# Optimization experiments

Measured on AMD Instinct MI355X. Metric: run time of the kernel, lower is better.

## Reference

```python
import jax, jax.numpy as jnp
import numpy as np

N = 500_000
H = 256
G = 4096
NUM_TIMESTEPS = 2


def setup_inputs() -> dict:
    key = jax.random.key(0)
    ks = jax.random.split(key, 12)
    s = 0.05
    x = jax.random.normal(ks[0], (N, H), dtype=jnp.float32)
    batch = jnp.sort(jax.random.randint(ks[1], (N,), 0, G, dtype=jnp.int64))
    return {
        "x": x,
        "gate_w1": jax.random.normal(ks[2], (H, H), dtype=jnp.float32) * s,
        "gate_b1": jax.random.normal(ks[3], (H,), dtype=jnp.float32) * s,
        "gate_w2": jax.random.normal(ks[4], (1, H), dtype=jnp.float32) * s,
        "gate_b2": jax.random.normal(ks[5], (1,), dtype=jnp.float32) * s,
        "gru_w_ih": jax.random.normal(ks[6], (3 * H, H), dtype=jnp.float32) * s,
        "gru_w_hh": jax.random.normal(ks[7], (3 * H, H), dtype=jnp.float32) * s,
        "gru_b_ih": jax.random.normal(ks[8], (3 * H,), dtype=jnp.float32) * s,
        "gru_b_hh": jax.random.normal(ks[9], (3 * H,), dtype=jnp.float32) * s,
        "batch": batch,
        "num_graphs": G,
    }


def _gru_cell(inp, h, w_ih, w_hh, b_ih, b_hh):
    # torch.nn.GRUCell semantics; gate order [r, z, n]
    gi = inp @ w_ih.T + b_ih
    gh = h @ w_hh.T + b_hh
    i_r, i_z, i_n = jnp.split(gi, 3, axis=-1)
    h_r, h_z, h_n = jnp.split(gh, 3, axis=-1)
    r = jax.nn.sigmoid(i_r + h_r)
    z = jax.nn.sigmoid(i_z + h_z)
    n = jnp.tanh(i_n + r * h_n)
    return (1.0 - z) * n + z * h


def reference(x, gate_w1, gate_b1, gate_w2, gate_b2,
              gru_w_ih, gru_w_hh, gru_b_ih, gru_b_hh,
              batch, num_graphs):
    counts = jax.ops.segment_sum(jnp.ones((x.shape[0],), x.dtype), batch,
                                 num_segments=num_graphs)
    denom = jnp.maximum(counts, 1.0)[:, None]  # empty graphs -> 0 mean

    def mean_pool(v):
        return jax.ops.segment_sum(v, batch, num_segments=num_graphs) / denom

    graph_repr = mean_pool(x)  # (G, H)
    for _ in range(NUM_TIMESTEPS):
        # gather per-node graph context (batch is sorted == node_to_graph)
        gate_input = x + graph_repr[batch]  # (N, H)
        hgate = jax.nn.relu(gate_input @ gate_w1.T + gate_b1)
        gate = jax.nn.sigmoid(hgate @ gate_w2.T + gate_b2)  # (N, 1)
        weighted_x = x * gate
        new_graph_repr = mean_pool(weighted_x)
        graph_repr = _gru_cell(new_graph_repr, graph_repr,
                               gru_w_ih, gru_w_hh, gru_b_ih, gru_b_hh)
        graph_repr = jax.nn.relu(graph_repr)
    return graph_repr
```

## Files before the change

kernel.cpp:

```cpp
#include <hip/hip_runtime.h>
#include <hip/hip_bf16.h>
#include <stdint.h>

#define H 256
#define G 4096
#define TK 32
#define TP0 128
#define TPB 256

typedef __attribute__((ext_vector_type(8))) short bf16x8;
typedef __attribute__((ext_vector_type(4))) float f32x4;
typedef __attribute__((ext_vector_type(2))) float f32x2;

__device__ inline short f2bf(float f){
  union { float f; uint32_t u; } v; v.f = f;
  uint32_t r = (v.u + 0x7FFFu + ((v.u >> 16) & 1u)) >> 16;
  return (short)(uint16_t)r;
}
__device__ inline float bf2f(short s){
  union { float f; uint32_t u; } v; v.u = ((uint32_t)(uint16_t)s) << 16;
  return v.f;
}
__device__ inline uint32_t pk2(float lo, float hi){
  return (uint32_t)(uint16_t)f2bf(lo) | ((uint32_t)(uint16_t)f2bf(hi) << 16);
}
__device__ inline uint32_t pkfp8(float4 v){
  int u = __builtin_amdgcn_cvt_pk_fp8_f32(v.x, v.y, 0, false);
  u = __builtin_amdgcn_cvt_pk_fp8_f32(v.z, v.w, u, true);
  return (uint32_t)u;
}
__device__ inline float sigmoidf_(float x){ return 1.f / (1.f + __expf(-x)); }

__device__ inline void ldsbar(){
  asm volatile("s_waitcnt lgkmcnt(0)" ::: "memory");
  __builtin_amdgcn_s_barrier();
}

__global__ void conv_w(const float* __restrict__ w1, const float* __restrict__ wih,
                       const float* __restrict__ whh,
                       short* __restrict__ o1, short* __restrict__ oih, short* __restrict__ ohh,
                       uint8_t* __restrict__ w1q,
                       float* __restrict__ counts, float* __restrict__ pool){
  int i = blockIdx.x * 256 + threadIdx.x;
  if (i < H*H) o1[i] = f2bf(w1[i]);
  if (i < 3*H*H){ oih[i] = f2bf(wih[i]); ohh[i] = f2bf(whh[i]); }
  if (i < H*H/4){
    float4 v = *(const float4*)(w1 + (size_t)i*4);
    *(uint32_t*)(w1q + (size_t)i*4) = pkfp8(v);
  }
  if (i < G) counts[i] = 0.f;
  for (int j = i; j < G*H; j += 768*256) pool[j] = 0.f;
}

__global__ __launch_bounds__(512) __attribute__((amdgpu_waves_per_eu(2, 8)))
void k0_pool(const float* __restrict__ x, const int* __restrict__ batch,
             float* __restrict__ pool, float* __restrict__ counts,
             uint8_t* __restrict__ xq, float* __restrict__ sgate, int nNodes){
  __shared__ int   ng[TP0];
  __shared__ float Pacc[8][H];
  __shared__ float Cacc[8];
  __shared__ int   spanSh;

  const int t = threadIdx.x;
  const int base = blockIdx.x * TP0;
  const int c4 = (t & 63) * 4;
  const int r0 = (t >> 6) * 16;

  float4 v[16];
  #pragma unroll
  for (int i = 0; i < 16; ++i){
    int node = base + r0 + i;
    if (node < nNodes) v[i] = *(const float4*)(x + (size_t)node*H + c4);
    else v[i] = make_float4(0.f,0.f,0.f,0.f);
  }

  { int gi = blockIdx.x * 512 + t; if (gi < nNodes) sgate[gi] = 0.f; }

  if (t < TP0) ng[t] = (base + t < nNodes) ? batch[base + t] : -1;
  for (int u = t; u < 8*H; u += 512) ((float*)Pacc)[u] = 0.f;
  if (t < 8) Cacc[t] = 0.f;
  __syncthreads();

  if (t == 0){
    int lg = ng[0];
    if (base + TP0 <= nNodes) lg = ng[TP0-1];
    else { for (int i = TP0-1; i > 0; --i){ if (ng[i] >= 0){ lg = ng[i]; break; } } }
    spanSh = (ng[0] >= 0) ? (lg - ng[0]) : -1;
  }

  if (xq){
    #pragma unroll
    for (int i = 0; i < 16; ++i){
      int node = base + r0 + i;
      if (node < nNodes)
        *(uint32_t*)(xq + (size_t)node*H + c4) = pkfp8(v[i]);
    }
  }
  __syncthreads();

  const int g0 = ng[0];
  const bool useLds = (spanSh >= 0) && (spanSh < 8);

  float ax=0.f, ay=0.f, az=0.f, aw=0.f;
  int cur = ng[r0];
  if (cur >= 0){
    #pragma unroll
    for (int i = 0; i < 16; ++i){
      int g = ng[r0 + i];
      if (g < 0) break;
      if (g != cur){
        if (useLds){
          atomicAdd(&Pacc[cur-g0][c4], ax);   atomicAdd(&Pacc[cur-g0][c4+1], ay);
          atomicAdd(&Pacc[cur-g0][c4+2], az); atomicAdd(&Pacc[cur-g0][c4+3], aw);
        } else {
          atomicAdd(&pool[(size_t)cur*H + c4], ax);   atomicAdd(&pool[(size_t)cur*H + c4+1], ay);
          atomicAdd(&pool[(size_t)cur*H + c4+2], az); atomicAdd(&pool[(size_t)cur*H + c4+3], aw);
        }
        ax=ay=az=aw=0.f; cur = g;
      }
      ax += v[i].x; ay += v[i].y; az += v[i].z; aw += v[i].w;
    }
    if (useLds){
      atomicAdd(&Pacc[cur-g0][c4], ax);   atomicAdd(&Pacc[cur-g0][c4+1], ay);
      atomicAdd(&Pacc[cur-g0][c4+2], az); atomicAdd(&Pacc[cur-g0][c4+3], aw);
    } else {
      atomicAdd(&pool[(size_t)cur*H + c4], ax);   atomicAdd(&pool[(size_t)cur*H + c4+1], ay);
      atomicAdd(&pool[(size_t)cur*H + c4+2], az); atomicAdd(&pool[(size_t)cur*H + c4+3], aw);
    }
  }
  if (t < TP0 && ng[t] >= 0){
    if (useLds) atomicAdd(&Cacc[ng[t]-g0], 1.f);
    else        atomicAdd(&counts[ng[t]], 1.f);
  }
  __syncthreads();

  if (useLds){
    int nr = spanSh + 1;
    for (int u = t; u < nr*H; u += 512){
      int r = u >> 8, c = u & 255;
      float vv = Pacc[r][c];
      if (vv != 0.f) atomicAdd(&pool[(size_t)(g0+r)*H + c], vv);
    }
    if (t < nr && Cacc[t] != 0.f) atomicAdd(&counts[g0 + t], Cacc[t]);
  }
}

__global__ __launch_bounds__(256) void kT2(float* __restrict__ pool,
    const float* __restrict__ counts, float* __restrict__ repr,
    const short* __restrict__ w1bf, const float* __restrict__ b1,
    uint32_t* __restrict__ hgp){
  __shared__ short Ar[16][H + 8];
  const int t    = threadIdx.x;
  const int wid  = t >> 6;
  const int lane = t & 63;
  const int l15  = lane & 15;
  const int l4   = lane >> 4;
  const int g0   = blockIdx.x * 16;

  for (int u = t; u < 16*32; u += 256){
    int row = u >> 5, cg = u & 31;
    int c0 = cg * 8;
    int g = g0 + row;
    float cnt = fmaxf(counts[g], 1.f);
    float4* pp = (float4*)(pool + (size_t)g*H + c0);
    float4 p0 = pp[0], p1 = pp[1];
    p0.x/=cnt; p0.y/=cnt; p0.z/=cnt; p0.w/=cnt;
    p1.x/=cnt; p1.y/=cnt; p1.z/=cnt; p1.w/=cnt;
    float4* rp = (float4*)(repr + (size_t)g*H + c0);
    rp[0] = p0; rp[1] = p1;
    pp[0] = make_float4(0.f,0.f,0.f,0.f);
    pp[1] = make_float4(0.f,0.f,0.f,0.f);
    bf16x8 o;
    o[0]=f2bf(p0.x); o[1]=f2bf(p0.y); o[2]=f2bf(p0.z); o[3]=f2bf(p0.w);
    o[4]=f2bf(p1.x); o[5]=f2bf(p1.y); o[6]=f2bf(p1.z); o[7]=f2bf(p1.w);
    *(bf16x8*)(&Ar[row][c0]) = o;
  }
  __syncthreads();

  f32x4 acc[4];
  #pragma unroll
  for (int i = 0; i < 4; ++i) acc[i] = (f32x4){0.f,0.f,0.f,0.f};
  #pragma unroll
  for (int kc = 0; kc < 8; ++kc){
    bf16x8 a = *(bf16x8*)(&Ar[l15][kc*32 + l4*8]);
    #pragma unroll
    for (int nt = 0; nt < 4; ++nt){
      int col = wid*64 + nt*16 + l15;
      bf16x8 b = *(const bf16x8*)(w1bf + (size_t)col*H + kc*32 + l4*8);
      acc[nt] = __builtin_amdgcn_mfma_f32_16x16x32_bf16(a, b, acc[nt], 0, 0, 0);
    }
  }
  const float b1v0 = b1[wid*64 + l15];
  const float b1v1 = b1[wid*64 + 16 + l15];
  const float b1v2 = b1[wid*64 + 32 + l15];
  const float b1v3 = b1[wid*64 + 48 + l15];
  #pragma unroll
  for (int j = 0; j < 4; ++j){
    int row = l4*4 + j;
    hgp[(size_t)(g0+row)*128 + wid*32 + l15]      = pk2(acc[0][j]+b1v0, acc[1][j]+b1v1);
    hgp[(size_t)(g0+row)*128 + wid*32 + 16 + l15] = pk2(acc[2][j]+b1v2, acc[3][j]+b1v3);
  }
}

__global__ __launch_bounds__(256) __attribute__((amdgpu_waves_per_eu(3, 4)))
void k1a_fp8(
    const uint8_t* __restrict__ xq, const int* __restrict__ batch,
    const uint32_t* __restrict__ hgp, const uint8_t* __restrict__ w1q,
    const float* __restrict__ w2, float* __restrict__ sgate,
    int nNodes, int nTiles, int nBlk){

  __shared__ uint8_t Ain[2][TK][H + 16];
  __shared__ int     ngS[2][TK];

  const int t    = threadIdx.x;
  const int wid  = t >> 6;
  const int lane = t & 63;
  const int l15  = lane & 15;
  const int l4   = lane >> 4;
  const int colB = wid*64;

  const int tile0 = (int)(((long long)blockIdx.x * nTiles) / nBlk);
  const int tile1 = (int)(((long long)(blockIdx.x+1) * nTiles) / nBlk);
  if (tile0 >= tile1) return;

  long BfA0[8], BfA1[8], BfB0[8], BfB1[8];
  {
    const uint8_t* wp = w1q + (size_t)(colB + l15)*H + l4*8;
    #pragma unroll
    for (int kc = 0; kc < 8; ++kc){
      BfA0[kc] = *(const long*)(wp + kc*32);
      BfA1[kc] = *(const long*)(wp + 16*H + kc*32);
      BfB0[kc] = *(const long*)(wp + 32*H + kc*32);
      BfB1[kc] = *(const long*)(wp + 48*H + kc*32);
    }
  }
  const float w2A0 = w2[colB + l15];
  const float w2A1 = w2[colB + 16 + l15];
  const float w2B0 = w2[colB + 32 + l15];
  const float w2B1 = w2[colB + 48 + l15];

  const int srow  = t >> 4;
  const int scolB = (t & 15) * 16;
  uint4 xv0, xv1;
  int ngv = -1;

  auto issueT = [&](int tile){
    int base = tile * TK;
    int n0 = base + srow, n1 = n0 + 16;
    xv0 = (n0 < nNodes) ? *(const uint4*)(xq + (size_t)n0*H + scolB) : make_uint4(0,0,0,0);
    xv1 = (n1 < nNodes) ? *(const uint4*)(xq + (size_t)n1*H + scolB) : make_uint4(0,0,0,0);
    if (t < TK){
      int node = base + t;
      ngv = (node < nNodes) ? batch[node] : -1;
    }
  };
  auto stageT = [&](int buf){
    *(uint4*)(&Ain[buf][srow][scolB])      = xv0;
    *(uint4*)(&Ain[buf][srow + 16][scolB]) = xv1;
    if (t < TK) ngS[buf][t] = ngv;
  };

  issueT(tile0);
  stageT(0);
  if (tile0 + 1 < tile1) issueT(tile0 + 1);

  int cur = 0;
  for (int tile = tile0; tile < tile1; ++tile, cur ^= 1){
    ldsbar();

    uint32_t hvp[2][4];
    #pragma unroll
    for (int r = 0; r < 2; ++r)
      #pragma unroll
      for (int j = 0; j < 4; ++j){
        int g = ngS[cur][r*16 + l4*4 + j];
        hvp[r][j] = (g >= 0) ? hgp[(size_t)g*128 + wid*32 + l15] : 0u;
      }

    f32x4 acc0[2], acc1[2];
    #pragma unroll
    for (int r = 0; r < 2; ++r){ acc0[r] = (f32x4){0.f,0.f,0.f,0.f}; acc1[r] = (f32x4){0.f,0.f,0.f,0.f}; }
    #pragma unroll
    for (int kc = 0; kc < 8; ++kc){
      #pragma unroll
      for (int r = 0; r < 2; ++r){
        long a = *(const long*)(&Ain[cur][r*16 + l15][kc*32 + l4*8]);
        acc0[r] = __builtin_amdgcn_mfma_f32_16x16x32_fp8_fp8(a, BfA0[kc], acc0[r], 0, 0, 0);
        acc1[r] = __builtin_amdgcn_mfma_f32_16x16x32_fp8_fp8(a, BfA1[kc], acc1[r], 0, 0, 0);
      }
    }

    if (tile + 1 < tile1){
      stageT(cur ^ 1);
      if (tile + 2 < tile1) issueT(tile + 2);
    }

    float p[2][4];
    #pragma unroll
    for (int r = 0; r < 2; ++r)
      #pragma unroll
      for (int j = 0; j < 4; ++j){
        float h0 = fmaxf(acc0[r][j] + bf2f((short)(uint16_t)(hvp[r][j] & 0xFFFFu)), 0.f);
        float h1 = fmaxf(acc1[r][j] + bf2f((short)(uint16_t)(hvp[r][j] >> 16)), 0.f);
        p[r][j] = w2A0*h0 + w2A1*h1;
      }

    #pragma unroll
    for (int r = 0; r < 2; ++r)
      #pragma unroll
      for (int j = 0; j < 4; ++j){
        int g = ngS[cur][r*16 + l4*4 + j];
        hvp[r][j] = (g >= 0) ? hgp[(size_t)g*128 + wid*32 + 16 + l15] : 0u;
      }
    #pragma unroll
    for (int r = 0; r < 2; ++r){ acc0[r] = (f32x4){0.f,0.f,0.f,0.f}; acc1[r] = (f32x4){0.f,0.f,0.f,0.f}; }
    #pragma unroll
    for (int kc = 0; kc < 8; ++kc){
      #pragma unroll
      for (int r = 0; r < 2; ++r){
        long a = *(const long*)(&Ain[cur][r*16 + l15][kc*32 + l4*8]);
        acc0[r] = __builtin_amdgcn_mfma_f32_16x16x32_fp8_fp8(a, BfB0[kc], acc0[r], 0, 0, 0);
        acc1[r] = __builtin_amdgcn_mfma_f32_16x16x32_fp8_fp8(a, BfB1[kc], acc1[r], 0, 0, 0);
      }
    }
    #pragma unroll
    for (int r = 0; r < 2; ++r)
      #pragma unroll
      for (int j = 0; j < 4; ++j){
        float h0 = fmaxf(acc0[r][j] + bf2f((short)(uint16_t)(hvp[r][j] & 0xFFFFu)), 0.f);
        float h1 = fmaxf(acc1[r][j] + bf2f((short)(uint16_t)(hvp[r][j] >> 16)), 0.f);
        p[r][j] += w2B0*h0 + w2B1*h1;
      }

    #pragma unroll
    for (int off = 1; off < 16; off <<= 1){
      #pragma unroll
      for (int r = 0; r < 2; ++r)
        #pragma unroll
        for (int j = 0; j < 4; ++j) p[r][j] += __shfl_xor(p[r][j], off);
    }
    if (l15 == 0){
      int base = tile * TK;
      #pragma unroll
      for (int r = 0; r < 2; ++r)
        #pragma unroll
        for (int j = 0; j < 4; ++j){
          int idx = r*16 + l4*4 + j;
          if (ngS[cur][idx] >= 0)
            atomicAdd(&sgate[base + idx], p[r][j]);
        }
    }
  }
}

__global__ __launch_bounds__(512) __attribute__((amdgpu_waves_per_eu(2, 8)))
void k1b_q8(
    const uint8_t* __restrict__ xq, const int* __restrict__ batch,
    float* __restrict__ sgate, const float* __restrict__ b2p,
    float* __restrict__ pool, int nNodes){

  __shared__ int   ng[TPB];
  __shared__ float gs[TPB];
  __shared__ float Pacc[8][H];
  __shared__ int   spanSh;

  const int t = threadIdx.x;
  const int base = blockIdx.x * TPB;
  const int c4 = (t & 63) * 4;
  const int r0 = (t >> 6) * 32;

  uint32_t u[32];
  #pragma unroll
  for (int i = 0; i < 32; ++i){
    int node = base + r0 + i;
    u[i] = (node < nNodes) ? *(const uint32_t*)(xq + (size_t)node*H + c4) : 0u;
  }

  const float b2v = b2p[0];
  {
    int node = base + t;
    if (t < TPB){
      if (node < nNodes){
        ng[t] = batch[node];
        gs[t] = sigmoidf_(sgate[node] + b2v);
        sgate[node] = 0.f;
      } else { ng[t] = -1; gs[t] = 0.f; }
    }
  }
  for (int w = t; w < 8*H; w += 512) ((float*)Pacc)[w] = 0.f;
  __syncthreads();

  if (t == 0){
    int lg = ng[0];
    if (base + TPB <= nNodes) lg = ng[TPB-1];
    else { for (int i = TPB-1; i > 0; --i){ if (ng[i] >= 0){ lg = ng[i]; break; } } }
    spanSh = (ng[0] >= 0) ? (lg - ng[0]) : -1;
  }
  __syncthreads();

  const int g0 = ng[0];
  const bool useLds = (spanSh >= 0) && (spanSh < 8);

  float ax=0.f, ay=0.f, az=0.f, aw=0.f;
  int cur = ng[r0];
  if (cur >= 0){
    #pragma unroll
    for (int i = 0; i < 32; ++i){
      int g = ng[r0 + i];
      if (g < 0) break;
      if (g != cur){
        if (useLds){
          atomicAdd(&Pacc[cur-g0][c4], ax);   atomicAdd(&Pacc[cur-g0][c4+1], ay);
          atomicAdd(&Pacc[cur-g0][c4+2], az); atomicAdd(&Pacc[cur-g0][c4+3], aw);
        } else {
          atomicAdd(&pool[(size_t)cur*H + c4], ax);   atomicAdd(&pool[(size_t)cur*H + c4+1], ay);
          atomicAdd(&pool[(size_t)cur*H + c4+2], az); atomicAdd(&pool[(size_t)cur*H + c4+3], aw);
        }
        ax=ay=az=aw=0.f; cur = g;
      }
      float gv = gs[r0 + i];
      f32x2 lo = __builtin_amdgcn_cvt_pk_f32_fp8((int)u[i], false);
      f32x2 hi = __builtin_amdgcn_cvt_pk_f32_fp8((int)u[i], true);
      ax += gv * lo[0]; ay += gv * lo[1];
      az += gv * hi[0]; aw += gv * hi[1];
    }
    if (useLds){
      atomicAdd(&Pacc[cur-g0][c4], ax);   atomicAdd(&Pacc[cur-g0][c4+1], ay);
      atomicAdd(&Pacc[cur-g0][c4+2], az); atomicAdd(&Pacc[cur-g0][c4+3], aw);
    } else {
      atomicAdd(&pool[(size_t)cur*H + c4], ax);   atomicAdd(&pool[(size_t)cur*H + c4+1], ay);
      atomicAdd(&pool[(size_t)cur*H + c4+2], az); atomicAdd(&pool[(size_t)cur*H + c4+3], aw);
    }
  }
  __syncthreads();

  if (useLds){
    int nr = spanSh + 1;
    for (int w = t; w < nr*H; w += 512){
      int r = w >> 8, c = w & 255;
      float vv = Pacc[r][c];
      if (vv != 0.f) atomicAdd(&pool[(size_t)(g0+r)*H + c], vv);
    }
  }
}

__global__ __launch_bounds__(256) __attribute__((amdgpu_waves_per_eu(3, 4)))
void k1a_gate_f32(
    const float* __restrict__ xf32, const int* __restrict__ batch,
    const uint32_t* __restrict__ hgp, const short* __restrict__ w1bf,
    const float* __restrict__ w2, float* __restrict__ sgate,
    int nNodes, int nTiles, int nChains){

  __shared__ short Ain[2][TK][H + 8];
  __shared__ int   ngS[2][TK];

  const int t    = threadIdx.x;
  const int wid  = t >> 6;
  const int lane = t & 63;
  const int l15  = lane & 15;
  const int l4   = lane >> 4;

  const int ch    = blockIdx.x >= nChains;
  const int chain = ch ? blockIdx.x - nChains : blockIdx.x;
  const int colB  = ch*128 + wid*32;
  const int hgcol = ch*64 + wid*16 + l15;

  const int tile0 = (int)(((long long)chain * nTiles) / nChains);
  const int tile1 = (int)(((long long)(chain+1) * nTiles) / nChains);
  if (tile0 >= tile1) return;

  bf16x8 Bf0[8], Bf1[8];
  {
    const short* wp0 = w1bf + (size_t)(colB + l15)*H + l4*8;
    #pragma unroll
    for (int kc = 0; kc < 8; ++kc){
      Bf0[kc] = *(const bf16x8*)(wp0 + kc*32);
      Bf1[kc] = *(const bf16x8*)(wp0 + 16*H + kc*32);
    }
  }
  const float w2v0 = w2[colB + l15];
  const float w2v1 = w2[colB + 16 + l15];

  const int srow = t >> 5;
  const int scol = (t & 31) * 8;
  float4 xf[4][2];
  int ngv = -1;

  auto issueT = [&](int tile){
    int base = tile * TK;
    #pragma unroll
    for (int q = 0; q < 4; ++q){
      int node = base + srow + q*8;
      if (node < nNodes){
        const float4* xp = (const float4*)(xf32 + (size_t)node*H + scol);
        xf[q][0] = xp[0]; xf[q][1] = xp[1];
      } else { xf[q][0] = make_float4(0.f,0.f,0.f,0.f); xf[q][1] = make_float4(0.f,0.f,0.f,0.f); }
    }
    if (t < TK){
      int node = base + t;
      ngv = (node < nNodes) ? batch[node] : -1;
    }
  };
  auto stageT = [&](int buf){
    #pragma unroll
    for (int q = 0; q < 4; ++q){
      bf16x8 o;
      float4 a = xf[q][0], c = xf[q][1];
      o[0]=f2bf(a.x); o[1]=f2bf(a.y); o[2]=f2bf(a.z); o[3]=f2bf(a.w);
      o[4]=f2bf(c.x); o[5]=f2bf(c.y); o[6]=f2bf(c.z); o[7]=f2bf(c.w);
      *(bf16x8*)(&Ain[buf][srow + q*8][scol]) = o;
    }
    if (t < TK) ngS[buf][t] = ngv;
  };

  issueT(tile0);
  stageT(0);
  if (tile0 + 1 < tile1) issueT(tile0 + 1);

  int cur = 0;
  for (int tile = tile0; tile < tile1; ++tile, cur ^= 1){
    ldsbar();

    int gr[2][4];
    uint32_t hvp[2][4];
    #pragma unroll
    for (int r = 0; r < 2; ++r)
      #pragma unroll
      for (int j = 0; j < 4; ++j){
        int g = ngS[cur][r*16 + l4*4 + j];
        gr[r][j] = g;
        hvp[r][j] = (g >= 0) ? hgp[(size_t)g*128 + hgcol] : 0u;
      }

    f32x4 acc0[2], acc1[2];
    #pragma unroll
    for (int r = 0; r < 2; ++r){ acc0[r] = (f32x4){0.f,0.f,0.f,0.f}; acc1[r] = (f32x4){0.f,0.f,0.f,0.f}; }
    #pragma unroll
    for (int kc = 0; kc < 8; ++kc){
      #pragma unroll
      for (int r = 0; r < 2; ++r){
        bf16x8 a = *(bf16x8*)(&Ain[cur][r*16 + l15][kc*32 + l4*8]);
        acc0[r] = __builtin_amdgcn_mfma_f32_16x16x32_bf16(a, Bf0[kc], acc0[r], 0, 0, 0);
        acc1[r] = __builtin_amdgcn_mfma_f32_16x16x32_bf16(a, Bf1[kc], acc1[r], 0, 0, 0);
      }
    }

    if (tile + 1 < tile1){
      stageT(cur ^ 1);
      if (tile + 2 < tile1) issueT(tile + 2);
    }

    float p[2][4];
    #pragma unroll
    for (int r = 0; r < 2; ++r)
      #pragma unroll
      for (int j = 0; j < 4; ++j){
        float h0 = fmaxf(acc0[r][j] + bf2f((short)(uint16_t)(hvp[r][j] & 0xFFFFu)), 0.f);
        float h1 = fmaxf(acc1[r][j] + bf2f((short)(uint16_t)(hvp[r][j] >> 16)), 0.f);
        p[r][j] = w2v0*h0 + w2v1*h1;
      }
    #pragma unroll
    for (int off = 1; off < 16; off <<= 1){
      #pragma unroll
      for (int r = 0; r < 2; ++r)
        #pragma unroll
        for (int j = 0; j < 4; ++j) p[r][j] += __shfl_xor(p[r][j], off);
    }
    if (l15 == 0){
      int base = tile * TK;
      #pragma unroll
      for (int r = 0; r < 2; ++r)
        #pragma unroll
        for (int j = 0; j < 4; ++j){
          if (gr[r][j] >= 0)
            atomicAdd(&sgate[base + r*16 + l4*4 + j], p[r][j]);
        }
    }
  }
}

__global__ __launch_bounds__(512) __attribute__((amdgpu_waves_per_eu(2, 8)))
void k1b_f32(
    const float* __restrict__ xf32, const int* __restrict__ batch,
    float* __restrict__ sgate, const float* __restrict__ b2p,
    float* __restrict__ pool, int nNodes){

  __shared__ int   ng[TP0];
  __shared__ float gs[TP0];
  __shared__ float Pacc[8][H];
  __shared__ int   spanSh;

  const int t = threadIdx.x;
  const int base = blockIdx.x * TP0;
  const int c4 = (t & 63) * 4;
  const int r0 = (t >> 6) * 16;

  float4 vf[16];
  #pragma unroll
  for (int i = 0; i < 16; ++i){
    int node = base + r0 + i;
    vf[i] = (node < nNodes) ? *(const float4*)(xf32 + (size_t)node*H + c4)
                            : make_float4(0.f,0.f,0.f,0.f);
  }

  const float b2v = b2p[0];
  if (t < TP0){
    int node = base + t;
    if (node < nNodes){
      ng[t] = batch[node];
      gs[t] = sigmoidf_(sgate[node] + b2v);
      sgate[node] = 0.f;
    } else { ng[t] = -1; gs[t] = 0.f; }
  }
  for (int w = t; w < 8*H; w += 512) ((float*)Pacc)[w] = 0.f;
  __syncthreads();

  if (t == 0){
    int lg = ng[0];
    if (base + TP0 <= nNodes) lg = ng[TP0-1];
    else { for (int i = TP0-1; i > 0; --i){ if (ng[i] >= 0){ lg = ng[i]; break; } } }
    spanSh = (ng[0] >= 0) ? (lg - ng[0]) : -1;
  }
  __syncthreads();

  const int g0 = ng[0];
  const bool useLds = (spanSh >= 0) && (spanSh < 8);

  float ax=0.f, ay=0.f, az=0.f, aw=0.f;
  int cur = ng[r0];
  if (cur >= 0){
    #pragma unroll
    for (int i = 0; i < 16; ++i){
      int g = ng[r0 + i];
      if (g < 0) break;
      if (g != cur){
        if (useLds){
          atomicAdd(&Pacc[cur-g0][c4], ax);   atomicAdd(&Pacc[cur-g0][c4+1], ay);
          atomicAdd(&Pacc[cur-g0][c4+2], az); atomicAdd(&Pacc[cur-g0][c4+3], aw);
        } else {
          atomicAdd(&pool[(size_t)cur*H + c4], ax);   atomicAdd(&pool[(size_t)cur*H + c4+1], ay);
          atomicAdd(&pool[(size_t)cur*H + c4+2], az); atomicAdd(&pool[(size_t)cur*H + c4+3], aw);
        }
        ax=ay=az=aw=0.f; cur = g;
      }
      float gv = gs[r0 + i];
      ax += gv * bf2f(f2bf(vf[i].x)); ay += gv * bf2f(f2bf(vf[i].y));
      az += gv * bf2f(f2bf(vf[i].z)); aw += gv * bf2f(f2bf(vf[i].w));
    }
    if (useLds){
      atomicAdd(&Pacc[cur-g0][c4], ax);   atomicAdd(&Pacc[cur-g0][c4+1], ay);
      atomicAdd(&Pacc[cur-g0][c4+2], az); atomicAdd(&Pacc[cur-g0][c4+3], aw);
    } else {
      atomicAdd(&pool[(size_t)cur*H + c4], ax);   atomicAdd(&pool[(size_t)cur*H + c4+1], ay);
      atomicAdd(&pool[(size_t)cur*H + c4+2], az); atomicAdd(&pool[(size_t)cur*H + c4+3], aw);
    }
  }
  __syncthreads();

  if (useLds){
    int nr = spanSh + 1;
    for (int w = t; w < nr*H; w += 512){
      int r = w >> 8, c = w & 255;
      float vv = Pacc[r][c];
      if (vv != 0.f) atomicAdd(&pool[(size_t)(g0+r)*H + c], vv);
    }
  }
}

__global__ __launch_bounds__(256) void k2_gru(float* __restrict__ pool,
    const float* __restrict__ counts, const float* __restrict__ repr_in,
    const short* __restrict__ wihbf, const short* __restrict__ whhbf,
    const float* __restrict__ bih, const float* __restrict__ bhh,
    float* __restrict__ repr_out,
    const short* __restrict__ w1bf, const float* __restrict__ b1,
    uint32_t* __restrict__ hgp, int doHg){

  __shared__ short Anew[16][H + 8];
  __shared__ short Aold[16][H + 8];
  __shared__ float hold[16][H];
  __shared__ float srz[16][2*H];
  __shared__ float sni[16][H];
  __shared__ float snh[16][H];

  const int t    = threadIdx.x;
  const int wid  = t >> 6;
  const int lane = t & 63;
  const int l15  = lane & 15;
  const int l4   = lane >> 4;
  const int g0   = blockIdx.x * 16;

  for (int u = t; u < 16*H; u += 256){
    int row = u >> 8, c = u & 255;
    int g = g0 + row;
    float cnt = fmaxf(counts[g], 1.f);
    float rin = repr_in[(size_t)g*H + c];
    float nr  = pool[(size_t)g*H + c] / cnt;
    pool[(size_t)g*H + c] = 0.f;
    Anew[row][c] = f2bf(nr);
    Aold[row][c] = f2bf(rin);
    hold[row][c] = rin;
  }
  __syncthreads();

  f32x4 ai[12], ah[12];
  #pragma unroll
  for (int i = 0; i < 12; ++i){ ai[i] = (f32x4){0.f,0.f,0.f,0.f}; ah[i] = (f32x4){0.f,0.f,0.f,0.f}; }

  for (int kc = 0; kc < 8; ++kc){
    bf16x8 an = *(bf16x8*)(&Anew[l15][kc*32 + l4*8]);
    bf16x8 ao = *(bf16x8*)(&Aold[l15][kc*32 + l4*8]);
    #pragma unroll
    for (int nt = 0; nt < 12; ++nt){
      int n = wid*192 + nt*16 + l15;
      bf16x8 bi = *(const bf16x8*)(wihbf + (size_t)n*H + kc*32 + l4*8);
      bf16x8 bh = *(const bf16x8*)(whhbf + (size_t)n*H + kc*32 + l4*8);
      ai[nt] = __builtin_amdgcn_mfma_f32_16x16x32_bf16(an, bi, ai[nt], 0, 0, 0);
      ah[nt] = __builtin_amdgcn_mfma_f32_16x16x32_bf16(ao, bh, ah[nt], 0, 0, 0);
    }
  }

  #pragma unroll
  for (int nt = 0; nt < 12; ++nt){
    int n = wid*192 + nt*16 + l15;
    float bi = bih[n], bh = bhh[n];
    #pragma unroll
    for (int r = 0; r < 4; ++r){
      int row = l4*4 + r;
      float si = ai[nt][r] + bi;
      float sh = ah[nt][r] + bh;
      if (n < 2*H) srz[row][n] = si + sh;
      else { sni[row][n - 2*H] = si; snh[row][n - 2*H] = sh; }
    }
  }
  __syncthreads();

  for (int u = t; u < 16*H; u += 256){
    int row = u >> 8, c = u & 255;
    float rr = sigmoidf_(srz[row][c]);
    float zz = sigmoidf_(srz[row][H + c]);
    float nn = tanhf(sni[row][c] + rr * snh[row][c]);
    float hv = (1.f - zz) * nn + zz * hold[row][c];
    float out = fmaxf(hv, 0.f);
    repr_out[(size_t)(g0 + row)*H + c] = out;
    Anew[row][c] = f2bf(out);
  }

  if (doHg){
    __syncthreads();
    f32x4 acc[4];
    #pragma unroll
    for (int i = 0; i < 4; ++i) acc[i] = (f32x4){0.f,0.f,0.f,0.f};
    #pragma unroll
    for (int kc = 0; kc < 8; ++kc){
      bf16x8 a = *(bf16x8*)(&Anew[l15][kc*32 + l4*8]);
      #pragma unroll
      for (int nt = 0; nt < 4; ++nt){
        int col = wid*64 + nt*16 + l15;
        bf16x8 b = *(const bf16x8*)(w1bf + (size_t)col*H + kc*32 + l4*8);
        acc[nt] = __builtin_amdgcn_mfma_f32_16x16x32_bf16(a, b, acc[nt], 0, 0, 0);
      }
    }
    const float b1v0 = b1[wid*64 + l15];
    const float b1v1 = b1[wid*64 + 16 + l15];
    const float b1v2 = b1[wid*64 + 32 + l15];
    const float b1v3 = b1[wid*64 + 48 + l15];
    #pragma unroll
    for (int j = 0; j < 4; ++j){
      int row = l4*4 + j;
      hgp[(size_t)(g0+row)*128 + wid*32 + l15]      = pk2(acc[0][j]+b1v0, acc[1][j]+b1v1);
      hgp[(size_t)(g0+row)*128 + wid*32 + 16 + l15] = pk2(acc[2][j]+b1v2, acc[3][j]+b1v3);
    }
  }
}

extern "C" void kernel_launch(void* const* d_in, const int* in_sizes, int n_in,
                              void* d_out, int out_size, void* d_ws, size_t ws_size,
                              hipStream_t stream){
  const float* x    = (const float*)d_in[0];
  const float* w1   = (const float*)d_in[1];
  const float* b1   = (const float*)d_in[2];
  const float* w2   = (const float*)d_in[3];
  const float* b2   = (const float*)d_in[4];
  const float* wih  = (const float*)d_in[5];
  const float* whh  = (const float*)d_in[6];
  const float* bih  = (const float*)d_in[7];
  const float* bhh  = (const float*)d_in[8];
  const int*   batch= (const int*)d_in[9];
  const int N = in_sizes[9];

  char* ws = (char*)d_ws;
  short* w1bf   = (short*)(ws + 0);
  short* wihbf  = (short*)(ws + (1u<<17));
  short* whhbf  = (short*)(ws + (1u<<19));
  float* counts = (float*)(ws + 917504);
  uint8_t* w1q  = (uint8_t*)(ws + 933888);
  float* pool   = (float*)(ws + (1u<<20));
  float* repr   = (float*)(ws + (1u<<20) + (1u<<22));
  float* sgate  = (float*)(ws + (9u<<20));
  uint32_t* hgp = (uint32_t*)(ws + (12u<<20));
  float* outp   = (float*)d_out;

  const size_t XQ_OFF = (size_t)16u << 20;
  const bool useXq = ws_size >= XQ_OFF + (size_t)N * H;
  uint8_t* xq = useXq ? (uint8_t*)(ws + XQ_OFF) : nullptr;

  const int nTiles32 = (N + TK - 1) / TK;
  const int nBlk1a  = 1024;
  const int nChainsF= 512;
  const int nBlkP   = (N + TP0 - 1) / TP0;
  const int nBlkQ   = (N + TPB - 1) / TPB;

  conv_w<<<768, 256, 0, stream>>>(w1, wih, whh, w1bf, wihbf, whhbf, w1q, counts, pool);
  k0_pool<<<nBlkP, 512, 0, stream>>>(x, batch, pool, counts, xq, sgate, N);
  kT2<<<G/16, 256, 0, stream>>>(pool, counts, repr, w1bf, b1, hgp);

  for (int ts = 0; ts < 2; ++ts){
    if (useXq){
      k1a_fp8<<<nBlk1a, 256, 0, stream>>>(xq, batch, hgp, w1q, w2, sgate, N, nTiles32, nBlk1a);
      k1b_q8<<<nBlkQ, 512, 0, stream>>>(xq, batch, sgate, b2, pool, N);
    } else {
      k1a_gate_f32<<<nChainsF*2, 256, 0, stream>>>(x, batch, hgp, w1bf, w2, sgate, N, nTiles32, nChainsF);
      k1b_f32<<<nBlkP, 512, 0, stream>>>(x, batch, sgate, b2, pool, N);
    }
    k2_gru<<<G/16, 256, 0, stream>>>(pool, counts, repr, wihbf, whhbf, bih, bhh,
                                     (ts == 0) ? repr : outp,
                                     w1bf, b1, hgp, (ts == 0) ? 1 : 0);
  }
}
```

Baseline: 588.5 us.

## Precompute x@W1 once and reuse across timesteps via linearity

Uses the linearity of (x + repr[batch]) @ W1^T to compute x@W1^T once per call into a bf16 buffer hx (N×256). Each timestep then adds the per-graph hg term, applies relu and the w2 dot product inside the pooling kernel, so the fp8 MFMA GEMM no longer runs twice. The column layout of hg is changed to interleaved pairs so it matches hx. The cost is a 256 MB bf16 intermediate that is written once and read twice, and a larger workspace requirement that gates whether this path is used at all.

```diff
diff --git a/kernel.cpp b/kernel.cpp
--- a/kernel.cpp
+++ b/kernel.cpp
@@ -148,7 +148,7 @@
 __global__ __launch_bounds__(256) void kT2(float* __restrict__ pool,
     const float* __restrict__ counts, float* __restrict__ repr,
     const short* __restrict__ w1bf, const float* __restrict__ b1,
-    uint32_t* __restrict__ hgp){
+    uint32_t* __restrict__ hgl){
   __shared__ short Ar[16][H + 8];
   const int t    = threadIdx.x;
   const int wid  = t >> 6;
@@ -180,37 +180,33 @@
   f32x4 acc[4];
   #pragma unroll
   for (int i = 0; i < 4; ++i) acc[i] = (f32x4){0.f,0.f,0.f,0.f};
+  const short* bp0 = w1bf + (size_t)(wid*64 + 2*l15)*H;
+  const short* bq0 = w1bf + (size_t)(wid*64 + 32 + 2*l15)*H;
   #pragma unroll
   for (int kc = 0; kc < 8; ++kc){
     bf16x8 a = *(bf16x8*)(&Ar[l15][kc*32 + l4*8]);
-    #pragma unroll
-    for (int nt = 0; nt < 4; ++nt){
-      int col = wid*64 + nt*16 + l15;
-      bf16x8 b = *(const bf16x8*)(w1bf + (size_t)col*H + kc*32 + l4*8);
-      acc[nt] = __builtin_amdgcn_mfma_f32_16x16x32_bf16(a, b, acc[nt], 0, 0, 0);
-    }
-  }
-  const float b1v0 = b1[wid*64 + l15];
-  const float b1v1 = b1[wid*64 + 16 + l15];
-  const float b1v2 = b1[wid*64 + 32 + l15];
-  const float b1v3 = b1[wid*64 + 48 + l15];
+    acc[0] = __builtin_amdgcn_mfma_f32_16x16x32_bf16(a, *(const bf16x8*)(bp0 + kc*32 + l4*8), acc[0], 0, 0, 0);
+    acc[1] = __builtin_amdgcn_mfma_f32_16x16x32_bf16(a, *(const bf16x8*)(bp0 + H + kc*32 + l4*8), acc[1], 0, 0, 0);
+    acc[2] = __builtin_amdgcn_mfma_f32_16x16x32_bf16(a, *(const bf16x8*)(bq0 + kc*32 + l4*8), acc[2], 0, 0, 0);
+    acc[3] = __builtin_amdgcn_mfma_f32_16x16x32_bf16(a, *(const bf16x8*)(bq0 + H + kc*32 + l4*8), acc[3], 0, 0, 0);
+  }
+  const float b1p0 = b1[wid*64 + 2*l15];
+  const float b1p1 = b1[wid*64 + 2*l15 + 1];
+  const float b1q0 = b1[wid*64 + 32 + 2*l15];
+  const float b1q1 = b1[wid*64 + 32 + 2*l15 + 1];
   #pragma unroll
   for (int j = 0; j < 4; ++j){
     int row = l4*4 + j;
-    hgp[(size_t)(g0+row)*128 + wid*32 + l15]      = pk2(acc[0][j]+b1v0, acc[1][j]+b1v1);
-    hgp[(size_t)(g0+row)*128 + wid*32 + 16 + l15] = pk2(acc[2][j]+b1v2, acc[3][j]+b1v3);
+    hgl[(size_t)(g0+row)*128 + wid*32 + l15]      = pk2(acc[0][j]+b1p0, acc[1][j]+b1p1);
+    hgl[(size_t)(g0+row)*128 + wid*32 + 16 + l15] = pk2(acc[2][j]+b1q0, acc[3][j]+b1q1);
   }
 }
 
 __global__ __launch_bounds__(256) __attribute__((amdgpu_waves_per_eu(3, 4)))
-void k1a_fp8(
-    const uint8_t* __restrict__ xq, const int* __restrict__ batch,
-    const uint32_t* __restrict__ hgp, const uint8_t* __restrict__ w1q,
-    const float* __restrict__ w2, float* __restrict__ sgate,
-    int nNodes, int nTiles, int nBlk){
+void kX_hx(const uint8_t* __restrict__ xq, const uint8_t* __restrict__ w1q,
+           uint32_t* __restrict__ hx, int nNodes, int nTiles, int nBlk){
 
   __shared__ uint8_t Ain[2][TK][H + 16];
-  __shared__ int     ngS[2][TK];
 
   const int t    = threadIdx.x;
   const int wid  = t >> 6;
@@ -223,41 +219,32 @@
   const int tile1 = (int)(((long long)(blockIdx.x+1) * nTiles) / nBlk);
   if (tile0 >= tile1) return;
 
-  long BfA0[8], BfA1[8], BfB0[8], BfB1[8];
+  long BfP0[8], BfP1[8], BfQ0[8], BfQ1[8];
   {
-    const uint8_t* wp = w1q + (size_t)(colB + l15)*H + l4*8;
+    const uint8_t* wp = w1q + (size_t)(colB + 2*l15)*H + l4*8;
+    const uint8_t* wq = w1q + (size_t)(colB + 32 + 2*l15)*H + l4*8;
     #pragma unroll
     for (int kc = 0; kc < 8; ++kc){
-      BfA0[kc] = *(const long*)(wp + kc*32);
-      BfA1[kc] = *(const long*)(wp + 16*H + kc*32);
-      BfB0[kc] = *(const long*)(wp + 32*H + kc*32);
-      BfB1[kc] = *(const long*)(wp + 48*H + kc*32);
-    }
-  }
-  const float w2A0 = w2[colB + l15];
-  const float w2A1 = w2[colB + 16 + l15];
-  const float w2B0 = w2[colB + 32 + l15];
-  const float w2B1 = w2[colB + 48 + l15];
+      BfP0[kc] = *(const long*)(wp + kc*32);
+      BfP1[kc] = *(const long*)(wp + H + kc*32);
+      BfQ0[kc] = *(const long*)(wq + kc*32);
+      BfQ1[kc] = *(const long*)(wq + H + kc*32);
+    }
+  }
 
   const int srow  = t >> 4;
   const int scolB = (t & 15) * 16;
   uint4 xv0, xv1;
-  int ngv = -1;
 
   auto issueT = [&](int tile){
     int base = tile * TK;
     int n0 = base + srow, n1 = n0 + 16;
     xv0 = (n0 < nNodes) ? *(const uint4*)(xq + (size_t)n0*H + scolB) : make_uint4(0,0,0,0);
     xv1 = (n1 < nNodes) ? *(const uint4*)(xq + (size_t)n1*H + scolB) : make_uint4(0,0,0,0);
-    if (t < TK){
-      int node = base + t;
-      ngv = (node < nNodes) ? batch[node] : -1;
-    }
   };
   auto stageT = [&](int buf){
     *(uint4*)(&Ain[buf][srow][scolB])      = xv0;
     *(uint4*)(&Ain[buf][srow + 16][scolB]) = xv1;
-    if (t < TK) ngS[buf][t] = ngv;
   };
 
   issueT(tile0);
@@ -267,26 +254,18 @@
   int cur = 0;
   for (int tile = tile0; tile < tile1; ++tile, cur ^= 1){
     ldsbar();
-
-    uint32_t hvp[2][4];
-    #pragma unroll
-    for (int r = 0; r < 2; ++r)
-      #pragma unroll
-      for (int j = 0; j < 4; ++j){
-        int g = ngS[cur][r*16 + l4*4 + j];
-        hvp[r][j] = (g >= 0) ? hgp[(size_t)g*128 + wid*32 + l15] : 0u;
-      }
-
-    f32x4 acc0[2], acc1[2];
-    #pragma unroll
-    for (int r = 0; r < 2; ++r){ acc0[r] = (f32x4){0.f,0.f,0.f,0.f}; acc1[r] = (f32x4){0.f,0.f,0.f,0.f}; }
+    const int nbase = tile * TK;
+
+    f32x4 a0[2], a1[2];
+    #pragma unroll
+    for (int r = 0; r < 2; ++r){ a0[r] = (f32x4){0.f,0.f,0.f,0.f}; a1[r] = (f32x4){0.f,0.f,0.f,0.f}; }
     #pragma unroll
     for (int kc = 0; kc < 8; ++kc){
       #pragma unroll
       for (int r = 0; r < 2; ++r){
         long a = *(const long*)(&Ain[cur][r*16 + l15][kc*32 + l4*8]);
-        acc0[r] = __builtin_amdgcn_mfma_f32_16x16x32_fp8_fp8(a, BfA0[kc], acc0[r], 0, 0, 0);
-        acc1[r] = __builtin_amdgcn_mfma_f32_16x16x32_fp8_fp8(a, BfA1[kc], acc1[r], 0, 0, 0);
+        a0[r] = __builtin_amdgcn_mfma_f32_16x16x32_fp8_fp8(a, BfP0[kc], a0[r], 0, 0, 0);
+        a1[r] = __builtin_amdgcn_mfma_f32_16x16x32_fp8_fp8(a, BfP1[kc], a1[r], 0, 0, 0);
       }
     }
 
@@ -295,72 +274,46 @@
       if (tile + 2 < tile1) issueT(tile + 2);
     }
 
-    float p[2][4];
     #pragma unroll
     for (int r = 0; r < 2; ++r)
       #pragma unroll
       for (int j = 0; j < 4; ++j){
-        float h0 = fmaxf(acc0[r][j] + bf2f((short)(uint16_t)(hvp[r][j] & 0xFFFFu)), 0.f);
-        float h1 = fmaxf(acc1[r][j] + bf2f((short)(uint16_t)(hvp[r][j] >> 16)), 0.f);
-        p[r][j] = w2A0*h0 + w2A1*h1;
-      }
-
-    #pragma unroll
-    for (int r = 0; r < 2; ++r)
-      #pragma unroll
-      for (int j = 0; j < 4; ++j){
-        int g = ngS[cur][r*16 + l4*4 + j];
-        hvp[r][j] = (g >= 0) ? hgp[(size_t)g*128 + wid*32 + 16 + l15] : 0u;
-      }
-    #pragma unroll
-    for (int r = 0; r < 2; ++r){ acc0[r] = (f32x4){0.f,0.f,0.f,0.f}; acc1[r] = (f32x4){0.f,0.f,0.f,0.f}; }
+        int node = nbase + r*16 + l4*4 + j;
+        if (node < nNodes)
+          hx[(size_t)node*128 + wid*32 + l15] = pk2(a0[r][j], a1[r][j]);
+      }
+
+    #pragma unroll
+    for (int r = 0; r < 2; ++r){ a0[r] = (f32x4){0.f,0.f,0.f,0.f}; a1[r] = (f32x4){0.f,0.f,0.f,0.f}; }
     #pragma unroll
     for (int kc = 0; kc < 8; ++kc){
       #pragma unroll
       for (int r = 0; r < 2; ++r){
         long a = *(const long*)(&Ain[cur][r*16 + l15][kc*32 + l4*8]);
-        acc0[r] = __builtin_amdgcn_mfma_f32_16x16x32_fp8_fp8(a, BfB0[kc], acc0[r], 0, 0, 0);
-        acc1[r] = __builtin_amdgcn_mfma_f32_16x16x32_fp8_fp8(a, BfB1[kc], acc1[r], 0, 0, 0);
+        a0[r] = __builtin_amdgcn_mfma_f32_16x16x32_fp8_fp8(a, BfQ0[kc], a0[r], 0, 0, 0);
+        a1[r] = __builtin_amdgcn_mfma_f32_16x16x32_fp8_fp8(a, BfQ1[kc], a1[r], 0, 0, 0);
       }
     }
     #pragma unroll
     for (int r = 0; r < 2; ++r)
       #pragma unroll
       for (int j = 0; j < 4; ++j){
-        float h0 = fmaxf(acc0[r][j] + bf2f((short)(uint16_t)(hvp[r][j] & 0xFFFFu)), 0.f);
-        float h1 = fmaxf(acc1[r][j] + bf2f((short)(uint16_t)(hvp[r][j] >> 16)), 0.f);
-        p[r][j] += w2B0*h0 + w2B1*h1;
-      }
-
-    #pragma unroll
-    for (int off = 1; off < 16; off <<= 1){
-      #pragma unroll
-      for (int r = 0; r < 2; ++r)
-        #pragma unroll
-        for (int j = 0; j < 4; ++j) p[r][j] += __shfl_xor(p[r][j], off);
-    }
-    if (l15 == 0){
-      int base = tile * TK;
-      #pragma unroll
-      for (int r = 0; r < 2; ++r)
-        #pragma unroll
-        for (int j = 0; j < 4; ++j){
-          int idx = r*16 + l4*4 + j;
-          if (ngS[cur][idx] >= 0)
-            atomicAdd(&sgate[base + idx], p[r][j]);
-        }
-    }
+        int node = nbase + r*16 + l4*4 + j;
+        if (node < nNodes)
+          hx[(size_t)node*128 + wid*32 + 16 + l15] = pk2(a0[r][j], a1[r][j]);
+      }
   }
 }
 
 __global__ __launch_bounds__(512) __attribute__((amdgpu_waves_per_eu(2, 8)))
-void k1b_q8(
-    const uint8_t* __restrict__ xq, const int* __restrict__ batch,
-    float* __restrict__ sgate, const float* __restrict__ b2p,
-    float* __restrict__ pool, int nNodes){
+void kG(const uint32_t* __restrict__ hx, const uint32_t* __restrict__ hgl,
+        const uint8_t* __restrict__ xq, const int* __restrict__ batch,
+        const float* __restrict__ w2, const float* __restrict__ b2p,
+        float* __restrict__ pool, int nNodes){
 
   __shared__ int   ng[TPB];
   __shared__ float gs[TPB];
+  __shared__ float w2s[H];
   __shared__ float Pacc[8][H];
   __shared__ int   spanSh;
 
@@ -377,16 +330,12 @@
   }
 
   const float b2v = b2p[0];
-  {
-    int node = base + t;
-    if (t < TPB){
-      if (node < nNodes){
-        ng[t] = batch[node];
-        gs[t] = sigmoidf_(sgate[node] + b2v);
-        sgate[node] = 0.f;
-      } else { ng[t] = -1; gs[t] = 0.f; }
-    }
-  }
+  const int nA = base + (t >> 1);
+  const int half = t & 1;
+  const int gA = (nA < nNodes) ? batch[nA] : -1;
+
+  if (t < H) w2s[t] = w2[t];
+  if (t < TPB) ng[t] = (base + t < nNodes) ? batch[base + t] : -1;
   for (int w = t; w < 8*H; w += 512) ((float*)Pacc)[w] = 0.f;
   __syncthreads();
 
@@ -396,6 +345,23 @@
     else { for (int i = TPB-1; i > 0; --i){ if (ng[i] >= 0){ lg = ng[i]; break; } } }
     spanSh = (ng[0] >= 0) ? (lg - ng[0]) : -1;
   }
+
+  float s = 0.f;
+  if (gA >= 0){
+    const uint32_t* hxp = hx  + (size_t)nA*128 + half*64;
+    const uint32_t* hgp = hgl + (size_t)gA*128 + half*64;
+    #pragma unroll
+    for (int k = 0; k < 64; ++k){
+      uint32_t hxd = hxp[k];
+      uint32_t hgd = hgp[k];
+      float lo = bf2f((short)(uint16_t)(hxd & 0xFFFFu)) + bf2f((short)(uint16_t)(hgd & 0xFFFFu));
+      float hi = bf2f((short)(uint16_t)(hxd >> 16))     + bf2f((short)(uint16_t)(hgd >> 16));
+      int c = half*128 + k*2;
+      s += w2s[c] * fmaxf(lo, 0.f) + w2s[c+1] * fmaxf(hi, 0.f);
+    }
+  }
+  s += __shfl_xor(s, 1);
+  if ((t & 1) == 0) gs[t >> 1] = (gA >= 0) ? sigmoidf_(s + b2v) : 0.f;
   __syncthreads();
 
   const int g0 = ng[0];
@@ -447,7 +413,7 @@
 __global__ __launch_bounds__(256) __attribute__((amdgpu_waves_per_eu(3, 4)))
 void k1a_gate_f32(
     const float* __restrict__ xf32, const int* __restrict__ batch,
-    const uint32_t* __restrict__ hgp, const short* __restrict__ w1bf,
+    const uint32_t* __restrict__ hgl, const short* __restrict__ w1bf,
     const float* __restrict__ w2, float* __restrict__ sgate,
     int nNodes, int nTiles, int nChains){
 
@@ -463,7 +429,7 @@
   const int ch    = blockIdx.x >= nChains;
   const int chain = ch ? blockIdx.x - nChains : blockIdx.x;
   const int colB  = ch*128 + wid*32;
-  const int hgcol = ch*64 + wid*16 + l15;
+  const int sel   = l15 & 1;
 
   const int tile0 = (int)(((long long)chain * nTiles) / nChains);
   const int tile1 = (int)(((long long)(chain+1) * nTiles) / nChains);
@@ -522,14 +488,19 @@
     ldsbar();
 
     int gr[2][4];
-    uint32_t hvp[2][4];
+    float hvA[2][4], hvB[2][4];
     #pragma unroll
     for (int r = 0; r < 2; ++r)
       #pragma unroll
       for (int j = 0; j < 4; ++j){
         int g = ngS[cur][r*16 + l4*4 + j];
         gr[r][j] = g;
-        hvp[r][j] = (g >= 0) ? hgp[(size_t)g*128 + hgcol] : 0u;
+        if (g >= 0){
+          uint32_t dA = hgl[(size_t)g*128 + (colB>>1) + (l15>>1)];
+          uint32_t dB = hgl[(size_t)g*128 + (colB>>1) + 8 + (l15>>1)];
+          hvA[r][j] = bf2f((short)(uint16_t)(sel ? (dA >> 16) : (dA & 0xFFFFu)));
+          hvB[r][j] = bf2f((short)(uint16_t)(sel ? (dB >> 16) : (dB & 0xFFFFu)));
+        } else { hvA[r][j] = 0.f; hvB[r][j] = 0.f; }
       }
 
     f32x4 acc0[2], acc1[2];
@@ -555,8 +526,8 @@
     for (int r = 0; r < 2; ++r)
       #pragma unroll
       for (int j = 0; j < 4; ++j){
-        float h0 = fmaxf(acc0[r][j] + bf2f((short)(uint16_t)(hvp[r][j] & 0xFFFFu)), 0.f);
-        float h1 = fmaxf(acc1[r][j] + bf2f((short)(uint16_t)(hvp[r][j] >> 16)), 0.f);
+        float h0 = fmaxf(acc0[r][j] + hvA[r][j], 0.f);
+        float h1 = fmaxf(acc1[r][j] + hvB[r][j], 0.f);
         p[r][j] = w2v0*h0 + w2v1*h1;
       }
     #pragma unroll
@@ -673,7 +644,7 @@
     const float* __restrict__ bih, const float* __restrict__ bhh,
     float* __restrict__ repr_out,
     const short* __restrict__ w1bf, const float* __restrict__ b1,
-    uint32_t* __restrict__ hgp, int doHg){
+    uint32_t* __restrict__ hgl, int doHg){
 
   __shared__ short Anew[16][H + 8];
   __shared__ short Aold[16][H + 8];
@@ -750,25 +721,25 @@
     f32x4 acc[4];
     #pragma unroll
     for (int i = 0; i < 4; ++i) acc[i] = (f32x4){0.f,0.f,0.f,0.f};
+    const short* bp0 = w1bf + (size_t)(wid*64 + 2*l15)*H;
+    const short* bq0 = w1bf + (size_t)(wid*64 + 32 + 2*l15)*H;
     #pragma unroll
     for (int kc = 0; kc < 8; ++kc){
       bf16x8 a = *(bf16x8*)(&Anew[l15][kc*32 + l4*8]);
-      #pragma unroll
-      for (int nt = 0; nt < 4; ++nt){
-        int col = wid*64 + nt*16 + l15;
-        bf16x8 b = *(const bf16x8*)(w1bf + (size_t)col*H + kc*32 + l4*8);
-        acc[nt] = __builtin_amdgcn_mfma_f32_16x16x32_bf16(a, b, acc[nt], 0, 0, 0);
-      }
-    }
-    const float b1v0 = b1[wid*64 + l15];
-    const float b1v1 = b1[wid*64 + 16 + l15];
-    const float b1v2 = b1[wid*64 + 32 + l15];
-    const float b1v3 = b1[wid*64 + 48 + l15];
+      acc[0] = __builtin_amdgcn_mfma_f32_16x16x32_bf16(a, *(const bf16x8*)(bp0 + kc*32 + l4*8), acc[0], 0, 0, 0);
+      acc[1] = __builtin_amdgcn_mfma_f32_16x16x32_bf16(a, *(const bf16x8*)(bp0 + H + kc*32 + l4*8), acc[1], 0, 0, 0);
+      acc[2] = __builtin_amdgcn_mfma_f32_16x16x32_bf16(a, *(const bf16x8*)(bq0 + kc*32 + l4*8), acc[2], 0, 0, 0);
+      acc[3] = __builtin_amdgcn_mfma_f32_16x16x32_bf16(a, *(const bf16x8*)(bq0 + H + kc*32 + l4*8), acc[3], 0, 0, 0);
+    }
+    const float b1p0 = b1[wid*64 + 2*l15];
+    const float b1p1 = b1[wid*64 + 2*l15 + 1];
+    const float b1q0 = b1[wid*64 + 32 + 2*l15];
+    const float b1q1 = b1[wid*64 + 32 + 2*l15 + 1];
     #pragma unroll
     for (int j = 0; j < 4; ++j){
       int row = l4*4 + j;
-      hgp[(size_t)(g0+row)*128 + wid*32 + l15]      = pk2(acc[0][j]+b1v0, acc[1][j]+b1v1);
-      hgp[(size_t)(g0+row)*128 + wid*32 + 16 + l15] = pk2(acc[2][j]+b1v2, acc[3][j]+b1v3);
+      hgl[(size_t)(g0+row)*128 + wid*32 + l15]      = pk2(acc[0][j]+b1p0, acc[1][j]+b1p1);
+      hgl[(size_t)(g0+row)*128 + wid*32 + 16 + l15] = pk2(acc[2][j]+b1q0, acc[3][j]+b1q1);
     }
   }
 }
@@ -797,33 +768,36 @@
   float* pool   = (float*)(ws + (1u<<20));
   float* repr   = (float*)(ws + (1u<<20) + (1u<<22));
   float* sgate  = (float*)(ws + (9u<<20));
-  uint32_t* hgp = (uint32_t*)(ws + (12u<<20));
+  uint32_t* hgl = (uint32_t*)(ws + (12u<<20));
   float* outp   = (float*)d_out;
 
   const size_t XQ_OFF = (size_t)16u << 20;
-  const bool useXq = ws_size >= XQ_OFF + (size_t)N * H;
-  uint8_t* xq = useXq ? (uint8_t*)(ws + XQ_OFF) : nullptr;
+  const size_t HX_OFF = XQ_OFF + ((size_t)128u << 20);
+  const bool useXq = ws_size >= HX_OFF + (size_t)N * 512;
+  uint8_t*  xq = useXq ? (uint8_t*)(ws + XQ_OFF) : nullptr;
+  uint32_t* hx = useXq ? (uint32_t*)(ws + HX_OFF) : nullptr;
 
   const int nTiles32 = (N + TK - 1) / TK;
-  const int nBlk1a  = 1024;
+  const int nBlkX   = 1024;
   const int nChainsF= 512;
   const int nBlkP   = (N + TP0 - 1) / TP0;
   const int nBlkQ   = (N + TPB - 1) / TPB;
 
   conv_w<<<768, 256, 0, stream>>>(w1, wih, whh, w1bf, wihbf, whhbf, w1q, counts, pool);
   k0_pool<<<nBlkP, 512, 0, stream>>>(x, batch, pool, counts, xq, sgate, N);
-  kT2<<<G/16, 256, 0, stream>>>(pool, counts, repr, w1bf, b1, hgp);
+  if (useXq)
+    kX_hx<<<nBlkX, 256, 0, stream>>>(xq, w1q, hx, N, nTiles32, nBlkX);
+  kT2<<<G/16, 256, 0, stream>>>(pool, counts, repr, w1bf, b1, hgl);
 
   for (int ts = 0; ts < 2; ++ts){
     if (useXq){
-      k1a_fp8<<<nBlk1a, 256, 0, stream>>>(xq, batch, hgp, w1q, w2, sgate, N, nTiles32, nBlk1a);
-      k1b_q8<<<nBlkQ, 512, 0, stream>>>(xq, batch, sgate, b2, pool, N);
+      kG<<<nBlkQ, 512, 0, stream>>>(hx, hgl, xq, batch, w2, b2, pool, N);
     } else {
-      k1a_gate_f32<<<nChainsF*2, 256, 0, stream>>>(x, batch, hgp, w1bf, w2, sgate, N, nTiles32, nChainsF);
+      k1a_gate_f32<<<nChainsF*2, 256, 0, stream>>>(x, batch, hgl, w1bf, w2, sgate, N, nTiles32, nChainsF);
       k1b_f32<<<nBlkP, 512, 0, stream>>>(x, batch, sgate, b2, pool, N);
     }
     k2_gru<<<G/16, 256, 0, stream>>>(pool, counts, repr, wihbf, whhbf, bih, bhh,
                                      (ts == 0) ? repr : outp,
-                                     w1bf, b1, hgp, (ts == 0) ? 1 : 0);
-  }
-}
+                                     w1bf, b1, hgl, (ts == 0) ? 1 : 0);
+  }
+}
```

Result: no change. 598.2 us (+1.6%).
